# Kernel optimization log

Measured on AMD Instinct MI355X. Metric: run time of the kernel, lower is better.

## Reference

```python
import jax, jax.numpy as jnp
import numpy as np

S = 64.0      # arcface scale
M = 0.5       # arcface angular margin
EPS = 1e-07


def setup_inputs() -> dict:
    key = jax.random.key(0)
    k1, k2, k3 = jax.random.split(key, 3)
    N, D, C = 1024, 512, 100000
    x = jax.random.normal(k1, (N, D), dtype=jnp.float32)
    W = jax.random.normal(k2, (C, D), dtype=jnp.float32)
    labels = jax.random.randint(k3, (N,), 0, C, dtype=jnp.int64)
    return {"x": x, "W": W, "labels": labels}


def reference(x, W, labels):
    # L2-normalize embeddings and class weights (rows)
    xn = x / jnp.linalg.norm(x, axis=1, keepdims=True)
    Wn = W / jnp.linalg.norm(W, axis=1, keepdims=True)
    # cosine logits: [N, C]
    wf = jnp.einsum('nd,cd->nc', xn, Wn)
    N = x.shape[0]
    target_cos = wf[jnp.arange(N), labels]  # [N]
    # arcface: s * cos(acos(clamp(cos)) + m)
    numerator = S * jnp.cos(jnp.arccos(jnp.clip(target_cos, -1.0 + EPS, 1.0 - EPS)) + M)
    # masked sum over non-target classes (replaces the per-sample torch.cat exclusion)
    onehot = jax.nn.one_hot(labels, wf.shape[1], dtype=jnp.bool_)
    excl_sum = jnp.sum(jnp.where(onehot, 0.0, jnp.exp(S * wf)), axis=1)  # [N]
    denominator = jnp.exp(numerator) + excl_sum
    L = numerator - jnp.log(denominator)
    return -jnp.mean(L)
```

## Files before the change

kernel.cpp:

```cpp
#include <hip/hip_runtime.h>
#include <hip/hip_bf16.h>

using f32x4 = __attribute__((ext_vector_type(4))) float;

#define DDIM 512
#define NROWS 1024
#define CCLS 100000
#define NCT 782
#define CPAD (NCT * 128)
#define NPADC ((float)(CPAD - CCLS))
#define GRID_BLOCKS 1024

#define XSCALE 92.33248261689366f

__device__ inline void gload_lds16(const void* g, void* l) {
    __builtin_amdgcn_global_load_lds(
        (const __attribute__((address_space(1))) void*)g,
        (__attribute__((address_space(3))) void*)l, 16, 0, 0);
}

__device__ inline unsigned int pk4_fp8(float a, float b, float c, float d) {
    int w = __builtin_amdgcn_cvt_pk_fp8_f32(a, b, 0, false);
    w = __builtin_amdgcn_cvt_pk_fp8_f32(c, d, w, true);
    return (unsigned int)w;
}

__global__ __launch_bounds__(256) void norm_x(const float* __restrict__ x,
                                              unsigned char* __restrict__ xf8) {
    const int row = blockIdx.x;
    const int tid = threadIdx.x;
    float2 v = *(const float2*)(x + (size_t)row * DDIM + tid * 2);
    float ss = v.x * v.x + v.y * v.y;
#pragma unroll
    for (int m = 1; m < 64; m <<= 1) ss += __shfl_xor(ss, m);
    __shared__ float wsum[4];
    if ((tid & 63) == 0) wsum[tid >> 6] = ss;
    __syncthreads();
    float inv = XSCALE / sqrtf(wsum[0] + wsum[1] + wsum[2] + wsum[3]);
    if (tid < 128) {
        float4 a = *(const float4*)(x + (size_t)row * DDIM + tid * 4);
        ((unsigned int*)xf8)[(size_t)row * (DDIM / 4) + tid] =
            pk4_fp8(a.x * inv, a.y * inv, a.z * inv, a.w * inv);
    }
}

__global__ __launch_bounds__(256) void norm_w_cvt(const float* __restrict__ W,
                                                  unsigned char* __restrict__ Wf8) {
    const int row  = blockIdx.x * 4 + (threadIdx.x >> 6);
    const int lane = threadIdx.x & 63;
    if (row < CCLS) {
        const float4* p = (const float4*)(W + (size_t)row * DDIM + lane * 8);
        float4 a = p[0], b = p[1];
        float ss = a.x*a.x + a.y*a.y + a.z*a.z + a.w*a.w
                 + b.x*b.x + b.y*b.y + b.z*b.z + b.w*b.w;
#pragma unroll
        for (int m = 1; m < 64; m <<= 1) ss += __shfl_xor(ss, m);
        float inv = (ss > 0.0f) ? (1.0f / sqrtf(ss)) : 0.0f;
        uint2 u = { pk4_fp8(a.x * inv, a.y * inv, a.z * inv, a.w * inv),
                    pk4_fp8(b.x * inv, b.y * inv, b.z * inv, b.w * inv) };
        *(uint2*)(Wf8 + (size_t)row * DDIM + lane * 8) = u;
    } else {
        *(uint2*)(Wf8 + (size_t)row * DDIM + lane * 8) = make_uint2(0u, 0u);
    }
}

__global__ __launch_bounds__(256) void target_dot(const float* __restrict__ x,
                                                  const float* __restrict__ W,
                                                  const int* __restrict__ labels,
                                                  float* __restrict__ tcos) {
    const int n    = blockIdx.x * 4 + (threadIdx.x >> 6);
    const int lane = threadIdx.x & 63;
    const int lab  = labels[n];
    const float4* px = (const float4*)(x + (size_t)n * DDIM + lane * 8);
    const float4* pw = (const float4*)(W + (size_t)lab * DDIM + lane * 8);
    float4 a0 = px[0], a1 = px[1], b0 = pw[0], b1 = pw[1];
    float xw = a0.x*b0.x + a0.y*b0.y + a0.z*b0.z + a0.w*b0.w
             + a1.x*b1.x + a1.y*b1.y + a1.z*b1.z + a1.w*b1.w;
    float xx = a0.x*a0.x + a0.y*a0.y + a0.z*a0.z + a0.w*a0.w
             + a1.x*a1.x + a1.y*a1.y + a1.z*a1.z + a1.w*a1.w;
    float ww = b0.x*b0.x + b0.y*b0.y + b0.z*b0.z + b0.w*b0.w
             + b1.x*b1.x + b1.y*b1.y + b1.z*b1.z + b1.w*b1.w;
#pragma unroll
    for (int m = 1; m < 64; m <<= 1) {
        xw += __shfl_xor(xw, m);
        xx += __shfl_xor(xx, m);
        ww += __shfl_xor(ww, m);
    }
    if (lane == 0) tcos[n] = xw / sqrtf(xx * ww);
}

__global__ __launch_bounds__(256, 4) void arc_gemm(
    const unsigned char* __restrict__ xf8,
    const unsigned char* __restrict__ Wf8,
    float* __restrict__ rowsum)
{
    __shared__ __align__(16) char lsA[128 * 128];
    __shared__ __align__(16) char lsW[128 * 128];
    __shared__ float lrow[128];

    const int tid  = threadIdx.x;
    const int lane = tid & 63;
    const int wid  = tid >> 6;
    const int wr   = wid >> 1, wc = wid & 1;
    const int q    = lane >> 4;
    const int fr   = lane & 15;

    const int grow = tid >> 3;
    const int gcol = ((tid & 7) ^ (grow & 7)) * 16;

    const int x    = blockIdx.x & 7;
    const int sidx = blockIdx.x >> 3;
    const int nct  = (NCT - 1 - x) / 8 + 1;
    const int npairs = nct * 8;

    for (int p = sidx; p < npairs; p += GRID_BLOCKS / 8) {
        const int c0 = (x + 8 * (p >> 3)) * 128;
        const int m0 = (p & 7) * 128;

        if (tid < 128) lrow[tid] = 0.0f;

        f32x4 acc[4][4];
#pragma unroll
        for (int i = 0; i < 4; ++i)
#pragma unroll
            for (int j = 0; j < 4; ++j) acc[i][j] = (f32x4)(0.0f);

#pragma unroll 1
        for (int k = 0; k < 4; ++k) {
            const int k0 = k * 128;
            __syncthreads();
#pragma unroll
            for (int it = 0; it < 4; ++it)
                gload_lds16(xf8 + (size_t)(m0 + it * 32 + grow) * DDIM + k0 + gcol,
                            lsA + (it * 256 + tid) * 16);
#pragma unroll
            for (int it = 0; it < 4; ++it)
                gload_lds16(Wf8 + (size_t)(c0 + it * 32 + grow) * DDIM + k0 + gcol,
                            lsW + (it * 256 + tid) * 16);
            __syncthreads();

#pragma unroll
            for (int ks = 0; ks < 4; ++ks) {
                const int kb = ks * 32 + q * 8;
                long af[4], bg[4];
#pragma unroll
                for (int i = 0; i < 4; ++i) {
                    int r = wr * 64 + i * 16 + fr;
                    af[i] = *(const long*)(lsA + r * 128 + (kb ^ ((r & 7) << 4)));
                }
#pragma unroll
                for (int j = 0; j < 4; ++j) {
                    int rc = wc * 64 + j * 16 + fr;
                    bg[j] = *(const long*)(lsW + rc * 128 + (kb ^ ((rc & 7) << 4)));
                }
#pragma unroll
                for (int i = 0; i < 4; ++i)
#pragma unroll
                    for (int j = 0; j < 4; ++j)
                        acc[i][j] = __builtin_amdgcn_mfma_f32_16x16x32_fp8_fp8(
                            af[i], bg[j], acc[i][j], 0, 0, 0);
            }
        }

#pragma unroll
        for (int i = 0; i < 4; ++i) {
#pragma unroll
            for (int v = 0; v < 4; ++v) {
                const int rl = wr * 64 + i * 16 + q * 4 + v;
                float sm = exp2f(acc[i][0][v]) + exp2f(acc[i][1][v])
                         + exp2f(acc[i][2][v]) + exp2f(acc[i][3][v]);
                sm += __shfl_xor(sm, 1);
                sm += __shfl_xor(sm, 2);
                sm += __shfl_xor(sm, 4);
                sm += __shfl_xor(sm, 8);
                if (fr == 0) atomicAdd(&lrow[rl], sm);
            }
        }
        __syncthreads();
        if (tid < 128) atomicAdd(&rowsum[m0 + tid], lrow[tid]);
    }
}

__global__ __launch_bounds__(256) void arc_final(const float* __restrict__ rowsum,
                                                 const float* __restrict__ tcos,
                                                 float* __restrict__ out) {
    const int tid = threadIdx.x;
    const float cosM = 0.87758256189037271612f;
    const float sinM = 0.47942553860420300027f;
    float L = 0.0f;
    for (int n = tid; n < NROWS; n += 256) {
        float tc  = tcos[n];
        float tcl = fminf(fmaxf(tc, -1.0f + 1e-7f), 1.0f - 1e-7f);
        float num = 64.0f * (tcl * cosM - sinM * sqrtf(fmaxf(0.0f, 1.0f - tcl * tcl)));
        float den = __expf(num) + (rowsum[n] - NPADC) - __expf(64.0f * tc);
        L += num - logf(den);
    }
    __shared__ float red[256];
    red[tid] = L;
    __syncthreads();
    for (int s = 128; s > 0; s >>= 1) {
        if (tid < s) red[tid] += red[tid + s];
        __syncthreads();
    }
    if (tid == 0) out[0] = -(red[0] / (float)NROWS);
}

extern "C" void kernel_launch(void* const* d_in, const int* in_sizes, int n_in,
                              void* d_out, int out_size, void* d_ws, size_t ws_size,
                              hipStream_t stream) {
    const float* x      = (const float*)d_in[0];
    const float* W      = (const float*)d_in[1];
    const int*   labels = (const int*)d_in[2];
    float* out = (float*)d_out;
    char*  ws  = (char*)d_ws;

    const size_t XF8_BYTES = (size_t)NROWS * DDIM;
    const size_t WF8_BYTES = (size_t)CPAD * DDIM;
    unsigned char* xf8 = (unsigned char*)(ws);
    unsigned char* Wf8 = (unsigned char*)(ws + XF8_BYTES);
    float* rowsum      = (float*)(ws + XF8_BYTES + WF8_BYTES);
    float* tcos        = (float*)(ws + XF8_BYTES + WF8_BYTES + 4096);

    (void)hipMemsetAsync(rowsum, 0, NROWS * sizeof(float), stream);

    norm_x<<<NROWS, 256, 0, stream>>>(x, xf8);
    norm_w_cvt<<<CPAD / 4, 256, 0, stream>>>(W, Wf8);
    target_dot<<<NROWS / 4, 256, 0, stream>>>(x, W, labels, tcos);

    arc_gemm<<<GRID_BLOCKS, 256, 0, stream>>>(xf8, Wf8, rowsum);

    arc_final<<<1, 256, 0, stream>>>(rowsum, tcos, out);
}
```

Before: 149.7 us.

## Use MI355 scaled 16x16x128 FP8 MFMA and fuse x normalization into target dot

Replaces four 16x16x32 FP8 MFMAs per k-chunk with a single gfx950 scaled 16x16x128 f8f6f4 MFMA using unit scales. Each lane now reads two 16-byte LDS fragments per operand instead of four 8-byte reads, which cuts issue count and LDS instructions in the GEMM inner loop. Separately, the x-normalization kernel is merged into the target-dot kernel, removing one launch and one pass over x. This relies on the K-order mapping of the new fragment layout matching between A and W, since the reduction is order-insensitive only if both operands are permuted identically.

New measurement: 139.8 us. 1.07x faster.

```diff
diff --git a/kernel.cpp b/kernel.cpp
--- a/kernel.cpp
+++ b/kernel.cpp
@@ -2,6 +2,8 @@
 #include <hip/hip_bf16.h>
 
 using f32x4 = __attribute__((ext_vector_type(4))) float;
+using i32x8 = __attribute__((ext_vector_type(8))) int;
+using u32x4 = __attribute__((ext_vector_type(4))) unsigned int;
 
 #define DDIM 512
 #define NROWS 1024
@@ -12,6 +14,7 @@
 #define GRID_BLOCKS 1024
 
 #define XSCALE 92.33248261689366f
+#define SCL1 0x7F7F7F7F
 
 __device__ inline void gload_lds16(const void* g, void* l) {
     __builtin_amdgcn_global_load_lds(
@@ -25,49 +28,20 @@
     return (unsigned int)w;
 }
 
-__global__ __launch_bounds__(256) void norm_x(const float* __restrict__ x,
-                                              unsigned char* __restrict__ xf8) {
-    const int row = blockIdx.x;
-    const int tid = threadIdx.x;
-    float2 v = *(const float2*)(x + (size_t)row * DDIM + tid * 2);
-    float ss = v.x * v.x + v.y * v.y;
-#pragma unroll
-    for (int m = 1; m < 64; m <<= 1) ss += __shfl_xor(ss, m);
-    __shared__ float wsum[4];
-    if ((tid & 63) == 0) wsum[tid >> 6] = ss;
-    __syncthreads();
-    float inv = XSCALE / sqrtf(wsum[0] + wsum[1] + wsum[2] + wsum[3]);
-    if (tid < 128) {
-        float4 a = *(const float4*)(x + (size_t)row * DDIM + tid * 4);
-        ((unsigned int*)xf8)[(size_t)row * (DDIM / 4) + tid] =
-            pk4_fp8(a.x * inv, a.y * inv, a.z * inv, a.w * inv);
-    }
-}
-
-__global__ __launch_bounds__(256) void norm_w_cvt(const float* __restrict__ W,
-                                                  unsigned char* __restrict__ Wf8) {
-    const int row  = blockIdx.x * 4 + (threadIdx.x >> 6);
-    const int lane = threadIdx.x & 63;
-    if (row < CCLS) {
-        const float4* p = (const float4*)(W + (size_t)row * DDIM + lane * 8);
-        float4 a = p[0], b = p[1];
-        float ss = a.x*a.x + a.y*a.y + a.z*a.z + a.w*a.w
-                 + b.x*b.x + b.y*b.y + b.z*b.z + b.w*b.w;
-#pragma unroll
-        for (int m = 1; m < 64; m <<= 1) ss += __shfl_xor(ss, m);
-        float inv = (ss > 0.0f) ? (1.0f / sqrtf(ss)) : 0.0f;
-        uint2 u = { pk4_fp8(a.x * inv, a.y * inv, a.z * inv, a.w * inv),
-                    pk4_fp8(b.x * inv, b.y * inv, b.z * inv, b.w * inv) };
-        *(uint2*)(Wf8 + (size_t)row * DDIM + lane * 8) = u;
-    } else {
-        *(uint2*)(Wf8 + (size_t)row * DDIM + lane * 8) = make_uint2(0u, 0u);
-    }
-}
-
-__global__ __launch_bounds__(256) void target_dot(const float* __restrict__ x,
-                                                  const float* __restrict__ W,
-                                                  const int* __restrict__ labels,
-                                                  float* __restrict__ tcos) {
+__device__ inline i32x8 read_frag128(const char* base, int row, int q) {
+    const int sw = row & 7;
+    u32x4 lo = *(const u32x4*)(base + row * 128 + (((2 * q)     ^ sw) << 4));
+    u32x4 hi = *(const u32x4*)(base + row * 128 + (((2 * q + 1) ^ sw) << 4));
+    i32x8 r = { (int)lo.x, (int)lo.y, (int)lo.z, (int)lo.w,
+                (int)hi.x, (int)hi.y, (int)hi.z, (int)hi.w };
+    return r;
+}
+
+__global__ __launch_bounds__(256) void prep_x(const float* __restrict__ x,
+                                              const float* __restrict__ W,
+                                              const int* __restrict__ labels,
+                                              unsigned char* __restrict__ xf8,
+                                              float* __restrict__ tcos) {
     const int n    = blockIdx.x * 4 + (threadIdx.x >> 6);
     const int lane = threadIdx.x & 63;
     const int lab  = labels[n];
@@ -86,7 +60,31 @@
         xx += __shfl_xor(xx, m);
         ww += __shfl_xor(ww, m);
     }
+    float inv = XSCALE * __frsqrt_rn(xx);
+    uint2 u = { pk4_fp8(a0.x * inv, a0.y * inv, a0.z * inv, a0.w * inv),
+                pk4_fp8(a1.x * inv, a1.y * inv, a1.z * inv, a1.w * inv) };
+    *(uint2*)(xf8 + (size_t)n * DDIM + lane * 8) = u;
     if (lane == 0) tcos[n] = xw / sqrtf(xx * ww);
+}
+
+__global__ __launch_bounds__(256) void norm_w_cvt(const float* __restrict__ W,
+                                                  unsigned char* __restrict__ Wf8) {
+    const int row  = blockIdx.x * 4 + (threadIdx.x >> 6);
+    const int lane = threadIdx.x & 63;
+    if (row < CCLS) {
+        const float4* p = (const float4*)(W + (size_t)row * DDIM + lane * 8);
+        float4 a = p[0], b = p[1];
+        float ss = a.x*a.x + a.y*a.y + a.z*a.z + a.w*a.w
+                 + b.x*b.x + b.y*b.y + b.z*b.z + b.w*b.w;
+#pragma unroll
+        for (int m = 1; m < 64; m <<= 1) ss += __shfl_xor(ss, m);
+        float inv = (ss > 0.0f) ? (1.0f / sqrtf(ss)) : 0.0f;
+        uint2 u = { pk4_fp8(a.x * inv, a.y * inv, a.z * inv, a.w * inv),
+                    pk4_fp8(b.x * inv, b.y * inv, b.z * inv, b.w * inv) };
+        *(uint2*)(Wf8 + (size_t)row * DDIM + lane * 8) = u;
+    } else {
+        *(uint2*)(Wf8 + (size_t)row * DDIM + lane * 8) = make_uint2(0u, 0u);
+    }
 }
 
 __global__ __launch_bounds__(256, 4) void arc_gemm(
@@ -139,26 +137,17 @@
                             lsW + (it * 256 + tid) * 16);
             __syncthreads();
 
-#pragma unroll
-            for (int ks = 0; ks < 4; ++ks) {
-                const int kb = ks * 32 + q * 8;
-                long af[4], bg[4];
-#pragma unroll
-                for (int i = 0; i < 4; ++i) {
-                    int r = wr * 64 + i * 16 + fr;
-                    af[i] = *(const long*)(lsA + r * 128 + (kb ^ ((r & 7) << 4)));
-                }
-#pragma unroll
-                for (int j = 0; j < 4; ++j) {
-                    int rc = wc * 64 + j * 16 + fr;
-                    bg[j] = *(const long*)(lsW + rc * 128 + (kb ^ ((rc & 7) << 4)));
-                }
-#pragma unroll
-                for (int i = 0; i < 4; ++i)
-#pragma unroll
-                    for (int j = 0; j < 4; ++j)
-                        acc[i][j] = __builtin_amdgcn_mfma_f32_16x16x32_fp8_fp8(
-                            af[i], bg[j], acc[i][j], 0, 0, 0);
+            i32x8 bg[4];
+#pragma unroll
+            for (int j = 0; j < 4; ++j)
+                bg[j] = read_frag128(lsW, wc * 64 + j * 16 + fr, q);
+#pragma unroll
+            for (int i = 0; i < 4; ++i) {
+                i32x8 af = read_frag128(lsA, wr * 64 + i * 16 + fr, q);
+#pragma unroll
+                for (int j = 0; j < 4; ++j)
+                    acc[i][j] = __builtin_amdgcn_mfma_scale_f32_16x16x128_f8f6f4(
+                        af, bg[j], acc[i][j], 0, 0, 0, SCL1, 0, SCL1);
             }
         }
 
@@ -223,9 +212,8 @@
 
     (void)hipMemsetAsync(rowsum, 0, NROWS * sizeof(float), stream);
 
-    norm_x<<<NROWS, 256, 0, stream>>>(x, xf8);
+    prep_x<<<NROWS / 4, 256, 0, stream>>>(x, W, labels, xf8, tcos);
     norm_w_cvt<<<CPAD / 4, 256, 0, stream>>>(W, Wf8);
-    target_dot<<<NROWS / 4, 256, 0, stream>>>(x, W, labels, tcos);
 
     arc_gemm<<<GRID_BLOCKS, 256, 0, stream>>>(xf8, Wf8, rowsum);
 
```
